# Optimization experiments

Hardware: AMD Instinct MI355X
Metric: run time of the kernel (lower is better)

## Reference

```python
import jax, jax.numpy as jnp
import numpy as np
from jax import lax

B_SZ, L, D_MODEL = 256, 4096, 4
D_STATE, D_CONV, EXPAND, OUT = 16, 4, 2, 3
D_INNER = EXPAND * D_MODEL  # 8
DT_RANK = max(1, -(-D_MODEL // 16))  # ceil(4/16) = 1


def setup_inputs() -> dict:
    key = jax.random.key(0)
    ks = jax.random.split(key, 12)
    s = 0.1
    x = jax.random.normal(ks[0], (B_SZ, L, D_MODEL), dtype=jnp.float32)
    W_in = jax.random.normal(ks[1], (2 * D_INNER, D_MODEL), jnp.float32) * s
    conv_w = jax.random.normal(ks[2], (D_INNER, 1, D_CONV), jnp.float32) * s
    conv_b = jax.random.normal(ks[3], (D_INNER,), jnp.float32) * s
    W_xproj = jax.random.normal(ks[4], (DT_RANK + 2 * D_STATE, D_INNER), jnp.float32) * s
    W_dt = jax.random.normal(ks[5], (D_INNER, DT_RANK), jnp.float32) * s
    b_dt = jax.random.normal(ks[6], (D_INNER,), jnp.float32) * s
    # standard Mamba S4D-real init: A = 1..N repeated per channel
    A_log = jnp.log(jnp.tile(jnp.arange(1, D_STATE + 1, dtype=jnp.float32)[None, :], (D_INNER, 1)))
    D = jnp.ones((D_INNER,), jnp.float32)
    W_out = jax.random.normal(ks[7], (D_MODEL, D_INNER), jnp.float32) * s
    fc_w = jax.random.normal(ks[8], (OUT, D_MODEL), jnp.float32) * s
    fc_b = jax.random.normal(ks[9], (OUT,), jnp.float32) * s
    return {"x": x, "W_in": W_in, "conv_w": conv_w, "conv_b": conv_b,
            "W_xproj": W_xproj, "W_dt": W_dt, "b_dt": b_dt, "A_log": A_log,
            "D": D, "W_out": W_out, "fc_w": fc_w, "fc_b": fc_b}


def _mamba_forward(x, W_in, conv_w, conv_b, W_xproj, W_dt, b_dt, A_log, D, W_out):
    # in_proj (no bias): (B,L,2*ed)
    xz = jnp.einsum('bld,ed->ble', x, W_in)
    xi, z = jnp.split(xz, 2, axis=-1)
    # depthwise causal conv1d over time
    xi_t = jnp.moveaxis(xi, 1, 2)  # (B, ed, L)
    xi_t = lax.conv_general_dilated(
        xi_t, conv_w, window_strides=(1,), padding=[(D_CONV - 1, 0)],
        feature_group_count=D_INNER, dimension_numbers=('NCH', 'OIH', 'NCH'))
    xi_t = xi_t + conv_b[None, :, None]
    u = jax.nn.silu(jnp.moveaxis(xi_t, 1, 2))  # (B, L, ed)
    # x_proj -> dt, B, C
    x_dbl = jnp.einsum('bld,rd->blr', u, W_xproj)
    dt_r = x_dbl[..., :DT_RANK]
    Bm = x_dbl[..., DT_RANK:DT_RANK + D_STATE]
    Cm = x_dbl[..., DT_RANK + D_STATE:]
    dt = jax.nn.softplus(jnp.einsum('blr,dr->bld', dt_r, W_dt) + b_dt)  # (B,L,ed)
    A = -jnp.exp(A_log)  # (ed, N)
    # selective scan over time
    def step(h, inp):
        dt_t, B_t, C_t, u_t = inp  # (B,ed),(B,N),(B,N),(B,ed)
        h = jnp.exp(dt_t[..., None] * A) * h + (dt_t * u_t)[..., None] * B_t[:, None, :]
        y = jnp.einsum('bdn,bn->bd', h, C_t)
        return h, y
    h0 = jnp.zeros((x.shape[0], D_INNER, D_STATE), x.dtype)
    inputs = (jnp.moveaxis(dt, 1, 0), jnp.moveaxis(Bm, 1, 0),
              jnp.moveaxis(Cm, 1, 0), jnp.moveaxis(u, 1, 0))
    _, ys = lax.scan(step, h0, inputs)  # (L,B,ed)
    y = jnp.moveaxis(ys, 0, 1) + u * D  # skip connection
    y = y * jax.nn.silu(z)
    return jnp.einsum('ble,de->bld', y, W_out)  # (B,L,d_model)


def reference(x, W_in, conv_w, conv_b, W_xproj, W_dt, b_dt, A_log, D, W_out, fc_w, fc_b):
    y = _mamba_forward(x, W_in, conv_w, conv_b, W_xproj, W_dt, b_dt, A_log, D, W_out)
    vel = jnp.einsum('bld,od->blo', y, fc_w) + fc_b  # (B,L,3)
    t = x[:, :, 0:1]
    dtm = t[:, 1:, :] - t[:, :-1, :]
    dtm = jnp.concatenate([jnp.zeros((x.shape[0], 1, 1), x.dtype), dtm], axis=1)
    return x[:, :, 1:4] + vel * dtm
```

## Files before the change

### kernel.cpp

```cpp
#include <hip/hip_runtime.h>
#include <hip/hip_fp16.h>

#define LSEQ   4096
#define SEG    1024
#define NCTOT  64
#define CLEN   64

__device__ __forceinline__ float rcpf(float v){ return __builtin_amdgcn_rcpf(v); }

template<int CTRL>
__device__ __forceinline__ float dppadd(float v){
  int r = __builtin_amdgcn_update_dpp(0, __builtin_bit_cast(int,v), CTRL, 0xF, 0xF, true);
  return v + __builtin_bit_cast(float,r);
}
__device__ __forceinline__ float quadsum(float v){
  v = dppadd<0xB1>(v);
  v = dppadd<0x4E>(v);
  return v;
}
__device__ __forceinline__ void qdt(float v, float& q, float& dt){
  float e = __expf(v);
  float qq = rcpf(1.f + e);
  q = qq;
  float d0 = -__logf(qq);
  dt = (v > 15.f) ? v : d0;
}
__device__ __forceinline__ float dot8(const float* __restrict__ w, const float* u){
  float s = 0.f;
  #pragma unroll
  for (int d=0; d<8; d++) s = fmaf(w[d], u[d], s);
  return s;
}
__device__ __forceinline__ float dot4v(const float* __restrict__ w, float4 v){
  return fmaf(w[0],v.x, fmaf(w[1],v.y, fmaf(w[2],v.z, w[3]*v.w)));
}
__device__ __forceinline__ float siluf(float v){ return v * rcpf(1.f + __expf(-v)); }

__global__ __launch_bounds__(256,4) void kA(
    const float* __restrict__ x, const float* __restrict__ W_in,
    const float* __restrict__ conv_w, const float* __restrict__ conv_b,
    const float* __restrict__ W_xproj, const float* __restrict__ W_dt,
    const float* __restrict__ b_dt,
    float* __restrict__ Ap, float* __restrict__ Hl)
{
  __shared__ float4 xs[SEG+4];
  __shared__ float2 Pl[4][16][10];
  __shared__ __half Bl[4][16][24];

  const int t = threadIdx.x;
  const int b  = blockIdx.x >> 2;
  const int qt = blockIdx.x & 3;
  const size_t base = (size_t)b*LSEQ + (size_t)qt*SEG;
  const float4* x4 = (const float4*)x;
  #pragma unroll
  for (int kk=0;kk<4;kk++) xs[3 + kk*256 + t] = x4[base + kk*256 + t];
  if (t < 3) xs[t] = (qt>0) ? x4[base - 3 + t] : make_float4(0.f,0.f,0.f,0.f);
  __syncthreads();

  const int w = t >> 6, lane = t & 63;
  const int pk = lane >> 4, pj = (lane >> 2) & 3, pp = lane & 3;
  const int sk = lane >> 4, sd = (lane >> 1) & 7, snh = lane & 1;

  float h[8]; float prun = 1.f;
  #pragma unroll
  for (int j=0;j<8;j++) h[j]=0.f;

  #pragma unroll 1
  for (int mt=0; mt<16; mt++){
    const int i0 = mt*4;
    {
      int rt = pk*4 + pj;
      int segrow = w*256 + pk*64 + i0 + pj;
      float4 v = xs[segrow + pp];
      float uu[8];
      #pragma unroll
      for (int d=0; d<8; d++){
        float xiw = dot4v(W_in + d*4, v);
        float s = quadsum(conv_w[d*4+pp] * xiw);
        uu[d] = siluf(s + conv_b[d]);
      }
      float bn[4];
      #pragma unroll
      for (int kd=0; kd<4; kd++) bn[kd] = dot8(W_xproj + (1+pp*4+kd)*8, uu);
      uint2 bw;
      ((__half2*)&bw)[0] = __floats2half2_rn(bn[0],bn[1]);
      ((__half2*)&bw)[1] = __floats2half2_rn(bn[2],bn[3]);
      *(uint2*)&Bl[w][rt][pp*4] = bw;
      float dtr = dot8(W_xproj, uu);
      int d0 = pp*2;
      float q0,dt0,q1,dt1;
      qdt(fmaf(dtr,W_dt[d0  ],b_dt[d0  ]), q0, dt0);
      qdt(fmaf(dtr,W_dt[d0+1],b_dt[d0+1]), q1, dt1);
      *(float4*)&Pl[w][rt][d0] = make_float4(q0, dt0*uu[d0], q1, dt1*uu[d0+1]);
    }
    {
      #pragma unroll
      for (int j=0;j<4;j++){
        int rt = sk*4 + j;
        float2 P = Pl[w][rt][sd];
        uint4 braw = *(uint4*)&Bl[w][rt][snh*8];
        float2 f0=__half22float2(((__half2*)&braw)[0]);
        float2 f1=__half22float2(((__half2*)&braw)[1]);
        float2 f2=__half22float2(((__half2*)&braw)[2]);
        float2 f3=__half22float2(((__half2*)&braw)[3]);
        float q=P.x, dtu=P.y;
        float q2=q*q, q4=q2*q2, q8=q4*q4;
        float p3=q2*q, p5=q4*q, p6=q4*q2, p7=p6*q;
        float m = snh ? q8 : 1.f;
        h[0]=fmaf(q *m, h[0], dtu*f0.x);
        h[1]=fmaf(q2*m, h[1], dtu*f0.y);
        h[2]=fmaf(p3*m, h[2], dtu*f1.x);
        h[3]=fmaf(q4*m, h[3], dtu*f1.y);
        h[4]=fmaf(p5*m, h[4], dtu*f2.x);
        h[5]=fmaf(p6*m, h[5], dtu*f2.y);
        h[6]=fmaf(p7*m, h[6], dtu*f3.x);
        h[7]=fmaf(q8*m, h[7], dtu*f3.y);
        prun *= q;
      }
    }
  }
  float Q=prun, Q2=Q*Q, Q4=Q2*Q2, Q8=Q4*Q4;
  float R3=Q2*Q, R5=Q4*Q, R6=Q4*Q2, R7=R6*Q;
  float M = snh ? Q8 : 1.f;
  size_t sb = ((size_t)(b*NCTOT + qt*16 + w*4 + sk))*128 + sd*16 + snh*8;
  *(float4*)&Ap[sb]   = make_float4(Q*M, Q2*M, R3*M, Q4*M);
  *(float4*)&Ap[sb+4] = make_float4(R5*M, R6*M, R7*M, Q8*M);
  *(float4*)&Hl[sb]   = make_float4(h[0],h[1],h[2],h[3]);
  *(float4*)&Hl[sb+4] = make_float4(h[4],h[5],h[6],h[7]);
}

__global__ __launch_bounds__(256) void kB(
    const float* __restrict__ Ap, const float* __restrict__ Hl,
    float* __restrict__ Hin)
{
  int g = blockIdx.x*256 + threadIdx.x;
  int b = g >> 7, e = g & 127;
  float h = 0.f;
  #pragma unroll 8
  for (int c=0; c<NCTOT; c++){
    size_t s = ((size_t)b*NCTOT + c)*128 + e;
    float a = Ap[s], hl = Hl[s];
    Hin[s] = h;
    h = fmaf(a, h, hl);
  }
}

__global__ __launch_bounds__(256,4) void kC(
    const float* __restrict__ x, const float* __restrict__ W_in,
    const float* __restrict__ conv_w, const float* __restrict__ conv_b,
    const float* __restrict__ W_xproj, const float* __restrict__ W_dt,
    const float* __restrict__ b_dt, const float* __restrict__ Dp,
    const float* __restrict__ W_out, const float* __restrict__ fc_w,
    const float* __restrict__ fc_b, const float* __restrict__ Hin,
    float* __restrict__ out)
{
  __shared__ float4  xs[SEG+4];
  __shared__ float2  Pl[4][16][10];
  __shared__ __half  BCl[4][16][40];
  __shared__ __half2 El[4][16][10];
  __shared__ float   yol[4][16][12];
  __shared__ __half  outStage[SEG*3];

  const int t = threadIdx.x;
  const int b  = blockIdx.x >> 2;
  const int qt = blockIdx.x & 3;
  const size_t base = (size_t)b*LSEQ + (size_t)qt*SEG;
  const float4* x4 = (const float4*)x;
  #pragma unroll
  for (int kk=0;kk<4;kk++) xs[3 + kk*256 + t] = x4[base + kk*256 + t];
  if (t < 3) xs[t] = (qt>0) ? x4[base - 3 + t] : make_float4(0.f,0.f,0.f,0.f);
  __syncthreads();

  const int w = t >> 6, lane = t & 63;
  const int pk = lane >> 4, pj = (lane >> 2) & 3, pp = lane & 3;
  const int sk = lane >> 4, sd = (lane >> 1) & 7, snh = lane & 1;
  const int eo = lane >> 4, err = lane & 15;

  float P2r[8]; float fb = 0.f;
  {
    int o = (eo < 3) ? eo : 0;
    #pragma unroll
    for (int d=0; d<8; d++){
      float s0 = 0.f;
      #pragma unroll
      for (int m=0;m<4;m++) s0 = fmaf(fc_w[o*4+m], W_out[m*8+d], s0);
      P2r[d] = s0;
    }
    fb = fc_b[o];
  }
  const float Dd0 = Dp[pp*2], Dd1 = Dp[pp*2+1];

  float h[8];
  {
    size_t sb = ((size_t)(b*NCTOT + qt*16 + w*4 + sk))*128 + sd*16 + snh*8;
    float4 h0 = *(const float4*)&Hin[sb];
    float4 h1 = *(const float4*)&Hin[sb+4];
    h[0]=h0.x;h[1]=h0.y;h[2]=h0.z;h[3]=h0.w;
    h[4]=h1.x;h[5]=h1.y;h[6]=h1.z;h[7]=h1.w;
  }

  #pragma unroll 1
  for (int mt=0; mt<16; mt++){
    const int i0 = mt*4;
    {
      int rt = pk*4 + pj;
      int segrow = w*256 + pk*64 + i0 + pj;
      float4 v = xs[segrow + pp];
      float uu[8];
      #pragma unroll
      for (int d=0; d<8; d++){
        float xiw = dot4v(W_in + d*4, v);
        float s = quadsum(conv_w[d*4+pp] * xiw);
        uu[d] = siluf(s + conv_b[d]);
      }
      float bn[4], cn[4];
      #pragma unroll
      for (int kd=0; kd<4; kd++){
        bn[kd] = dot8(W_xproj + ( 1+pp*4+kd)*8, uu);
        cn[kd] = dot8(W_xproj + (17+pp*4+kd)*8, uu);
      }
      uint2 bw, cw;
      ((__half2*)&bw)[0] = __floats2half2_rn(bn[0],bn[1]);
      ((__half2*)&bw)[1] = __floats2half2_rn(bn[2],bn[3]);
      ((__half2*)&cw)[0] = __floats2half2_rn(cn[0],cn[1]);
      ((__half2*)&cw)[1] = __floats2half2_rn(cn[2],cn[3]);
      *(uint2*)&BCl[w][rt][pp*4]      = bw;
      *(uint2*)&BCl[w][rt][16+pp*4]   = cw;
      float dtr = dot8(W_xproj, uu);
      float4 xc = xs[segrow + 3];
      int d0 = pp*2;
      float q0,dt0,q1,dt1;
      qdt(fmaf(dtr,W_dt[d0  ],b_dt[d0  ]), q0, dt0);
      qdt(fmaf(dtr,W_dt[d0+1],b_dt[d0+1]), q1, dt1);
      float z0 = dot4v(W_in + (8+d0  )*4, xc);
      float z1 = dot4v(W_in + (8+d0+1)*4, xc);
      float sz0 = siluf(z0), sz1 = siluf(z1);
      uint2 ew;
      ((__half2*)&ew)[0] = __floats2half2_rn(sz0, uu[d0  ]*Dd0*sz0);
      ((__half2*)&ew)[1] = __floats2half2_rn(sz1, uu[d0+1]*Dd1*sz1);
      *(uint2*)&El[w][rt][d0] = ew;
      *(float4*)&Pl[w][rt][d0] = make_float4(q0, dt0*uu[d0], q1, dt1*uu[d0+1]);
    }
    {
      #pragma unroll
      for (int j=0;j<4;j++){
        int rt = sk*4 + j;
        float2 P = Pl[w][rt][sd];
        uint4 braw = *(uint4*)&BCl[w][rt][snh*8];
        uint4 craw = *(uint4*)&BCl[w][rt][16+snh*8];
        float2 f0=__half22float2(((__half2*)&braw)[0]);
        float2 f1=__half22float2(((__half2*)&braw)[1]);
        float2 f2=__half22float2(((__half2*)&braw)[2]);
        float2 f3=__half22float2(((__half2*)&braw)[3]);
        float2 g0=__half22float2(((__half2*)&craw)[0]);
        float2 g1=__half22float2(((__half2*)&craw)[1]);
        float2 g2=__half22float2(((__half2*)&craw)[2]);
        float2 g3=__half22float2(((__half2*)&craw)[3]);
        float q=P.x, dtu=P.y;
        float q2=q*q, q4=q2*q2, q8=q4*q4;
        float p3=q2*q, p5=q4*q, p6=q4*q2, p7=p6*q;
        float m = snh ? q8 : 1.f;
        h[0]=fmaf(q *m, h[0], dtu*f0.x);
        h[1]=fmaf(q2*m, h[1], dtu*f0.y);
        h[2]=fmaf(p3*m, h[2], dtu*f1.x);
        h[3]=fmaf(q4*m, h[3], dtu*f1.y);
        h[4]=fmaf(p5*m, h[4], dtu*f2.x);
        h[5]=fmaf(p6*m, h[5], dtu*f2.y);
        h[6]=fmaf(p7*m, h[6], dtu*f3.x);
        h[7]=fmaf(q8*m, h[7], dtu*f3.y);
        float y = h[0]*g0.x;
        y = fmaf(h[1],g0.y,y); y = fmaf(h[2],g1.x,y); y = fmaf(h[3],g1.y,y);
        y = fmaf(h[4],g2.x,y); y = fmaf(h[5],g2.y,y); y = fmaf(h[6],g3.x,y);
        y = fmaf(h[7],g3.y,y);
        y = dppadd<0xB1>(y);
        if (!snh){
          float2 e = __half22float2(El[w][rt][sd]);
          yol[w][rt][sd] = fmaf(y, e.x, e.y);
        }
      }
    }
    if (lane < 48){
      int kk = err >> 2, jj = err & 3;
      float4 y0 = *(float4*)&yol[w][err][0];
      float4 y1 = *(float4*)&yol[w][err][4];
      float a = fb;
      a = fmaf(P2r[0],y0.x,a); a = fmaf(P2r[1],y0.y,a);
      a = fmaf(P2r[2],y0.z,a); a = fmaf(P2r[3],y0.w,a);
      a = fmaf(P2r[4],y1.x,a); a = fmaf(P2r[5],y1.y,a);
      a = fmaf(P2r[6],y1.z,a); a = fmaf(P2r[7],y1.w,a);
      int segrow = w*256 + kk*64 + i0 + jj;
      outStage[segrow*3 + eo] = __float2half(a);
    }
  }

  const float* xsf = (const float*)xs;
  float* outg = out + (size_t)(b*LSEQ + qt*SEG)*3;
  #pragma unroll
  for (int rep=0; rep<12; rep++){
    int gg = w*768 + rep*64 + lane;
    int row = gg/3;
    int o = gg - row*3;
    float acc = __half2float(outStage[gg]);
    float dtm = (qt==0 && row==0) ? 0.f : xsf[(3+row)*4] - xsf[(2+row)*4];
    float xc = xsf[(3+row)*4 + 1 + o];
    outg[gg] = fmaf(acc, dtm, xc);
  }
}

extern "C" void kernel_launch(void* const* d_in, const int* in_sizes, int n_in,
                              void* d_out, int out_size, void* d_ws, size_t ws_size,
                              hipStream_t stream)
{
  const float* x       = (const float*)d_in[0];
  const float* W_in    = (const float*)d_in[1];
  const float* conv_w  = (const float*)d_in[2];
  const float* conv_b  = (const float*)d_in[3];
  const float* W_xproj = (const float*)d_in[4];
  const float* W_dt    = (const float*)d_in[5];
  const float* b_dt    = (const float*)d_in[6];
  const float* Dp      = (const float*)d_in[8];
  const float* W_out   = (const float*)d_in[9];
  const float* fc_w    = (const float*)d_in[10];
  const float* fc_b    = (const float*)d_in[11];
  float* out = (float*)d_out;

  char* wsp = (char*)d_ws;
  float* Ap  = (float*)(wsp);
  float* Hl  = (float*)(wsp + (size_t)8388608);
  float* Hin = (float*)(wsp + (size_t)16777216);

  hipLaunchKernelGGL(kA, dim3(1024), dim3(256), 0, stream,
                     x, W_in, conv_w, conv_b, W_xproj, W_dt, b_dt, Ap, Hl);
  hipLaunchKernelGGL(kB, dim3(128), dim3(256), 0, stream, Ap, Hl, Hin);
  hipLaunchKernelGGL(kC, dim3(1024), dim3(256), 0, stream,
                     x, W_in, conv_w, conv_b, W_xproj, W_dt, b_dt, Dp,
                     W_out, fc_w, fc_b, Hin, out);
}
```

Before: 208.0 us.

## Halve chunk length, double grid, use packed float2 math and fp32 LDS staging

Segments shrink from 1024 to 512 timesteps and chunks from 64 to 32, so both scan kernels launch twice as many blocks and the middle chunk-carry kernel walks 128 chunks instead of 64. The per-step math is rewritten with two-wide vector types so it can map to packed FMA. The conv output is computed once per lane pair and broadcast with DPP rather than recomputed for all 8 channels per lane. B/C staging in LDS moves from half to float, and the silu(z) and D terms are stored with the dt data in one float4. The goal is more parallelism and fewer VALU instructions per step, at the cost of a longer serial carry pass, twice the workspace traffic, and more LDS per block.

```diff
diff --git a/kernel.cpp b/kernel.cpp
--- a/kernel.cpp
+++ b/kernel.cpp
@@ -2,41 +2,82 @@
 #include <hip/hip_fp16.h>
 
 #define LSEQ   4096
-#define SEG    1024
-#define NCTOT  64
-#define CLEN   64
+#define SEG    512
+#define CLEN   32
+#define NCTOT  128
+#define MTS    8
+
+typedef float v2f __attribute__((ext_vector_type(2)));
 
 __device__ __forceinline__ float rcpf(float v){ return __builtin_amdgcn_rcpf(v); }
 
 template<int CTRL>
-__device__ __forceinline__ float dppadd(float v){
-  int r = __builtin_amdgcn_update_dpp(0, __builtin_bit_cast(int,v), CTRL, 0xF, 0xF, true);
-  return v + __builtin_bit_cast(float,r);
-}
-__device__ __forceinline__ float quadsum(float v){
-  v = dppadd<0xB1>(v);
-  v = dppadd<0x4E>(v);
+__device__ __forceinline__ float dppmov(float v){
+  return __builtin_bit_cast(float, __builtin_amdgcn_update_dpp(0, __builtin_bit_cast(int,v), CTRL, 0xF, 0xF, true));
+}
+template<int CTRL>
+__device__ __forceinline__ v2f dppmov2(v2f v){
+  v2f r; r.x = dppmov<CTRL>(v.x); r.y = dppmov<CTRL>(v.y); return r;
+}
+__device__ __forceinline__ v2f fma2(v2f a, v2f b, v2f c){ return __builtin_elementwise_fma(a,b,c); }
+__device__ __forceinline__ v2f sp2(float x){ return (v2f){x,x}; }
+__device__ __forceinline__ v2f qsum2(v2f v){
+  v2f a = dppmov2<0xB1>(v); v += a;
+  v2f b2 = dppmov2<0x4E>(v); v += b2;
   return v;
 }
-__device__ __forceinline__ void qdt(float v, float& q, float& dt){
-  float e = __expf(v);
-  float qq = rcpf(1.f + e);
-  q = qq;
-  float d0 = -__logf(qq);
-  dt = (v > 15.f) ? v : d0;
-}
-__device__ __forceinline__ float dot8(const float* __restrict__ w, const float* u){
-  float s = 0.f;
-  #pragma unroll
-  for (int d=0; d<8; d++) s = fmaf(w[d], u[d], s);
-  return s;
-}
-__device__ __forceinline__ float dot4v(const float* __restrict__ w, float4 v){
-  return fmaf(w[0],v.x, fmaf(w[1],v.y, fmaf(w[2],v.z, w[3]*v.w)));
-}
-__device__ __forceinline__ float siluf(float v){ return v * rcpf(1.f + __expf(-v)); }
-
-__global__ __launch_bounds__(256,4) void kA(
+__device__ __forceinline__ v2f silu2(v2f v){
+  v2f s; s.x = rcpf(1.f+__expf(-v.x)); s.y = rcpf(1.f+__expf(-v.y));
+  return v*s;
+}
+__device__ __forceinline__ void qdt2(v2f vv, v2f& q, v2f& dt){
+  q.x = rcpf(1.f + __expf(vv.x));
+  q.y = rcpf(1.f + __expf(vv.y));
+  dt.x = (vv.x > 15.f) ? vv.x : -__logf(q.x);
+  dt.y = (vv.y > 15.f) ? vv.y : -__logf(q.y);
+}
+__device__ __forceinline__ float dot8p(const float* __restrict__ w, v2f u01, v2f u23, v2f u45, v2f u67){
+  const v2f* W = (const v2f*)w;
+  v2f a = W[0]*u01;
+  a = fma2(W[1], u23, a);
+  a = fma2(W[2], u45, a);
+  a = fma2(W[3], u67, a);
+  return a.x + a.y;
+}
+
+struct UU { v2f u01,u23,u45,u67, upair; float4 v; };
+__device__ __forceinline__ UU conv_u(const float4* __restrict__ xs, int segrow, int pp,
+    const float* __restrict__ W_in, const v2f* cwp, v2f cbp)
+{
+  float4 v = xs[segrow + pp];
+  v2f pre[4];
+  #pragma unroll
+  for (int dp=0; dp<4; dp++){
+    const float* wa = W_in + (2*dp)*4;
+    const float* wb = W_in + (2*dp+1)*4;
+    v2f a = (v2f){wa[0],wb[0]} * sp2(v.x);
+    a = fma2((v2f){wa[1],wb[1]}, sp2(v.y), a);
+    a = fma2((v2f){wa[2],wb[2]}, sp2(v.z), a);
+    a = fma2((v2f){wa[3],wb[3]}, sp2(v.w), a);
+    pre[dp] = a * cwp[dp];
+  }
+  #pragma unroll
+  for (int dp=0; dp<4; dp++) pre[dp] = qsum2(pre[dp]);
+  v2f c01 = (pp&1) ? pre[1] : pre[0];
+  v2f c23 = (pp&1) ? pre[3] : pre[2];
+  v2f own = (pp&2) ? c23 : c01;
+  own += cbp;
+  v2f up = silu2(own);
+  UU r;
+  r.u01 = dppmov2<0x00>(up);
+  r.u23 = dppmov2<0x55>(up);
+  r.u45 = dppmov2<0xAA>(up);
+  r.u67 = dppmov2<0xFF>(up);
+  r.upair = up; r.v = v;
+  return r;
+}
+
+__global__ __launch_bounds__(256,8) void kA(
     const float* __restrict__ x, const float* __restrict__ W_in,
     const float* __restrict__ conv_w, const float* __restrict__ conv_b,
     const float* __restrict__ W_xproj, const float* __restrict__ W_dt,
@@ -45,88 +86,86 @@
 {
   __shared__ float4 xs[SEG+4];
   __shared__ float2 Pl[4][16][10];
-  __shared__ __half Bl[4][16][24];
+  __shared__ float  Bs[4][16][20];
 
   const int t = threadIdx.x;
-  const int b  = blockIdx.x >> 2;
-  const int qt = blockIdx.x & 3;
+  const int b  = blockIdx.x >> 3;
+  const int qt = blockIdx.x & 7;
   const size_t base = (size_t)b*LSEQ + (size_t)qt*SEG;
   const float4* x4 = (const float4*)x;
-  #pragma unroll
-  for (int kk=0;kk<4;kk++) xs[3 + kk*256 + t] = x4[base + kk*256 + t];
+  xs[3 + t] = x4[base + t];
+  xs[3 + 256 + t] = x4[base + 256 + t];
   if (t < 3) xs[t] = (qt>0) ? x4[base - 3 + t] : make_float4(0.f,0.f,0.f,0.f);
   __syncthreads();
 
   const int w = t >> 6, lane = t & 63;
-  const int pk = lane >> 4, pj = (lane >> 2) & 3, pp = lane & 3;
-  const int sk = lane >> 4, sd = (lane >> 1) & 7, snh = lane & 1;
-
-  float h[8]; float prun = 1.f;
-  #pragma unroll
-  for (int j=0;j<8;j++) h[j]=0.f;
+  const int pk = lane>>4, pj=(lane>>2)&3, pp=lane&3;
+  const int sk = lane>>4, sd=(lane>>1)&7, snh=lane&1;
+  const int d0 = pp*2;
+
+  v2f cwp[4];
+  #pragma unroll
+  for (int dp=0;dp<4;dp++) cwp[dp] = (v2f){conv_w[(2*dp)*4+pp], conv_w[(2*dp+1)*4+pp]};
+  const v2f cbp  = (v2f){conv_b[d0], conv_b[d0+1]};
+  const v2f wdtp = (v2f){W_dt[d0], W_dt[d0+1]};
+  const v2f bdtp = (v2f){b_dt[d0], b_dt[d0+1]};
+
+  v2f h01=sp2(0.f), h23=sp2(0.f), h45=sp2(0.f), h67=sp2(0.f);
+  float prun = 1.f;
 
   #pragma unroll 1
-  for (int mt=0; mt<16; mt++){
-    const int i0 = mt*4;
+  for (int mt=0; mt<MTS; mt++){
     {
       int rt = pk*4 + pj;
-      int segrow = w*256 + pk*64 + i0 + pj;
-      float4 v = xs[segrow + pp];
-      float uu[8];
-      #pragma unroll
-      for (int d=0; d<8; d++){
-        float xiw = dot4v(W_in + d*4, v);
-        float s = quadsum(conv_w[d*4+pp] * xiw);
-        uu[d] = siluf(s + conv_b[d]);
-      }
+      int segrow = w*128 + pk*32 + mt*4 + pj;
+      UU s = conv_u(xs, segrow, pp, W_in, cwp, cbp);
       float bn[4];
       #pragma unroll
-      for (int kd=0; kd<4; kd++) bn[kd] = dot8(W_xproj + (1+pp*4+kd)*8, uu);
-      uint2 bw;
-      ((__half2*)&bw)[0] = __floats2half2_rn(bn[0],bn[1]);
-      ((__half2*)&bw)[1] = __floats2half2_rn(bn[2],bn[3]);
-      *(uint2*)&Bl[w][rt][pp*4] = bw;
-      float dtr = dot8(W_xproj, uu);
-      int d0 = pp*2;
-      float q0,dt0,q1,dt1;
-      qdt(fmaf(dtr,W_dt[d0  ],b_dt[d0  ]), q0, dt0);
-      qdt(fmaf(dtr,W_dt[d0+1],b_dt[d0+1]), q1, dt1);
-      *(float4*)&Pl[w][rt][d0] = make_float4(q0, dt0*uu[d0], q1, dt1*uu[d0+1]);
-    }
-    {
-      #pragma unroll
-      for (int j=0;j<4;j++){
-        int rt = sk*4 + j;
-        float2 P = Pl[w][rt][sd];
-        uint4 braw = *(uint4*)&Bl[w][rt][snh*8];
-        float2 f0=__half22float2(((__half2*)&braw)[0]);
-        float2 f1=__half22float2(((__half2*)&braw)[1]);
-        float2 f2=__half22float2(((__half2*)&braw)[2]);
-        float2 f3=__half22float2(((__half2*)&braw)[3]);
-        float q=P.x, dtu=P.y;
-        float q2=q*q, q4=q2*q2, q8=q4*q4;
-        float p3=q2*q, p5=q4*q, p6=q4*q2, p7=p6*q;
-        float m = snh ? q8 : 1.f;
-        h[0]=fmaf(q *m, h[0], dtu*f0.x);
-        h[1]=fmaf(q2*m, h[1], dtu*f0.y);
-        h[2]=fmaf(p3*m, h[2], dtu*f1.x);
-        h[3]=fmaf(q4*m, h[3], dtu*f1.y);
-        h[4]=fmaf(p5*m, h[4], dtu*f2.x);
-        h[5]=fmaf(p6*m, h[5], dtu*f2.y);
-        h[6]=fmaf(p7*m, h[6], dtu*f3.x);
-        h[7]=fmaf(q8*m, h[7], dtu*f3.y);
-        prun *= q;
-      }
-    }
-  }
-  float Q=prun, Q2=Q*Q, Q4=Q2*Q2, Q8=Q4*Q4;
-  float R3=Q2*Q, R5=Q4*Q, R6=Q4*Q2, R7=R6*Q;
-  float M = snh ? Q8 : 1.f;
-  size_t sb = ((size_t)(b*NCTOT + qt*16 + w*4 + sk))*128 + sd*16 + snh*8;
-  *(float4*)&Ap[sb]   = make_float4(Q*M, Q2*M, R3*M, Q4*M);
-  *(float4*)&Ap[sb+4] = make_float4(R5*M, R6*M, R7*M, Q8*M);
-  *(float4*)&Hl[sb]   = make_float4(h[0],h[1],h[2],h[3]);
-  *(float4*)&Hl[sb+4] = make_float4(h[4],h[5],h[6],h[7]);
+      for (int k2=0;k2<4;k2++)
+        bn[k2] = dot8p(W_xproj + (1+pp*4+k2)*8, s.u01,s.u23,s.u45,s.u67);
+      *(float4*)&Bs[w][rt][pp*4] = make_float4(bn[0],bn[1],bn[2],bn[3]);
+      float dtr = dot8p(W_xproj, s.u01,s.u23,s.u45,s.u67);
+      v2f q, dt;
+      qdt2(fma2(sp2(dtr), wdtp, bdtp), q, dt);
+      v2f dtu = dt * s.upair;
+      *(float4*)&Pl[w][rt][d0] = make_float4(q.x, dtu.x, q.y, dtu.y);
+    }
+    #pragma unroll
+    for (int j=0;j<4;j++){
+      int rt = sk*4 + j;
+      float2 P  = *(const float2*)&Pl[w][rt][sd];
+      float4 bA = *(const float4*)&Bs[w][rt][snh*8];
+      float4 bB = *(const float4*)&Bs[w][rt][snh*8+4];
+      float q = P.x, q2 = q*q;
+      v2f t01 = (v2f){q, q2};
+      v2f t23 = t01 * sp2(q2);
+      float q4 = t23.y;
+      v2f t45 = t01 * sp2(q4);
+      v2f t67 = t23 * sp2(q4);
+      float m = snh ? t67.y : 1.f;
+      v2f ms = sp2(m), du = sp2(P.y);
+      h01 = fma2(t01*ms, h01, du*(v2f){bA.x,bA.y});
+      h23 = fma2(t23*ms, h23, du*(v2f){bA.z,bA.w});
+      h45 = fma2(t45*ms, h45, du*(v2f){bB.x,bB.y});
+      h67 = fma2(t67*ms, h67, du*(v2f){bB.z,bB.w});
+      prun *= q;
+    }
+  }
+  float Q = prun, Q2 = Q*Q;
+  v2f s01 = (v2f){Q, Q2};
+  v2f s23 = s01 * sp2(Q2);
+  float Q4 = s23.y;
+  v2f s45 = s01 * sp2(Q4);
+  v2f s67 = s23 * sp2(Q4);
+  float M = snh ? s67.y : 1.f;
+  v2f Ms = sp2(M);
+  s01*=Ms; s23*=Ms; s45*=Ms; s67*=Ms;
+  int c = qt*16 + w*4 + sk;
+  size_t sb = ((size_t)(b*NCTOT + c))*128 + sd*16 + snh*8;
+  *(float4*)&Ap[sb]   = make_float4(s01.x,s01.y,s23.x,s23.y);
+  *(float4*)&Ap[sb+4] = make_float4(s45.x,s45.y,s67.x,s67.y);
+  *(float4*)&Hl[sb]   = make_float4(h01.x,h01.y,h23.x,h23.y);
+  *(float4*)&Hl[sb+4] = make_float4(h45.x,h45.y,h67.x,h67.y);
 }
 
 __global__ __launch_bounds__(256) void kB(
@@ -138,14 +177,14 @@
   float h = 0.f;
   #pragma unroll 8
   for (int c=0; c<NCTOT; c++){
-    size_t s = ((size_t)b*NCTOT + c)*128 + e;
+    size_t s = ((size_t)(b*NCTOT + c))*128 + e;
     float a = Ap[s], hl = Hl[s];
     Hin[s] = h;
     h = fmaf(a, h, hl);
   }
 }
 
-__global__ __launch_bounds__(256,4) void kC(
+__global__ __launch_bounds__(256,5) void kC(
     const float* __restrict__ x, const float* __restrict__ W_in,
     const float* __restrict__ conv_w, const float* __restrict__ conv_b,
     const float* __restrict__ W_xproj, const float* __restrict__ W_dt,
@@ -154,156 +193,148 @@
     const float* __restrict__ fc_b, const float* __restrict__ Hin,
     float* __restrict__ out)
 {
-  __shared__ float4  xs[SEG+4];
-  __shared__ float2  Pl[4][16][10];
-  __shared__ __half  BCl[4][16][40];
-  __shared__ __half2 El[4][16][10];
-  __shared__ float   yol[4][16][12];
-  __shared__ __half  outStage[SEG*3];
+  __shared__ float4 xs[SEG+4];
+  __shared__ float4 Pl4[4][16][9];
+  __shared__ float  BC[4][16][36];
+  __shared__ float  yol[4][16][8];
+  __shared__ __half outStage[SEG*3];
 
   const int t = threadIdx.x;
-  const int b  = blockIdx.x >> 2;
-  const int qt = blockIdx.x & 3;
+  const int b  = blockIdx.x >> 3;
+  const int qt = blockIdx.x & 7;
   const size_t base = (size_t)b*LSEQ + (size_t)qt*SEG;
   const float4* x4 = (const float4*)x;
-  #pragma unroll
-  for (int kk=0;kk<4;kk++) xs[3 + kk*256 + t] = x4[base + kk*256 + t];
+  xs[3 + t] = x4[base + t];
+  xs[3 + 256 + t] = x4[base + 256 + t];
   if (t < 3) xs[t] = (qt>0) ? x4[base - 3 + t] : make_float4(0.f,0.f,0.f,0.f);
   __syncthreads();
 
   const int w = t >> 6, lane = t & 63;
-  const int pk = lane >> 4, pj = (lane >> 2) & 3, pp = lane & 3;
-  const int sk = lane >> 4, sd = (lane >> 1) & 7, snh = lane & 1;
+  const int pk = lane>>4, pj=(lane>>2)&3, pp=lane&3;
+  const int sk = lane>>4, sd=(lane>>1)&7, snh=lane&1;
   const int eo = lane >> 4, err = lane & 15;
-
-  float P2r[8]; float fb = 0.f;
+  const int d0 = pp*2;
+
+  v2f cwp[4];
+  #pragma unroll
+  for (int dp=0;dp<4;dp++) cwp[dp] = (v2f){conv_w[(2*dp)*4+pp], conv_w[(2*dp+1)*4+pp]};
+  const v2f cbp  = (v2f){conv_b[d0], conv_b[d0+1]};
+  const v2f wdtp = (v2f){W_dt[d0], W_dt[d0+1]};
+  const v2f bdtp = (v2f){b_dt[d0], b_dt[d0+1]};
+  const v2f Dpp  = (v2f){Dp[d0], Dp[d0+1]};
+
+  v2f P2p[4]; float fb;
   {
     int o = (eo < 3) ? eo : 0;
+    float P2[8];
     #pragma unroll
     for (int d=0; d<8; d++){
       float s0 = 0.f;
       #pragma unroll
       for (int m=0;m<4;m++) s0 = fmaf(fc_w[o*4+m], W_out[m*8+d], s0);
-      P2r[d] = s0;
-    }
+      P2[d] = s0;
+    }
+    P2p[0]=(v2f){P2[0],P2[1]}; P2p[1]=(v2f){P2[2],P2[3]};
+    P2p[2]=(v2f){P2[4],P2[5]}; P2p[3]=(v2f){P2[6],P2[7]};
     fb = fc_b[o];
   }
-  const float Dd0 = Dp[pp*2], Dd1 = Dp[pp*2+1];
-
-  float h[8];
+
+  v2f h01, h23, h45, h67;
   {
-    size_t sb = ((size_t)(b*NCTOT + qt*16 + w*4 + sk))*128 + sd*16 + snh*8;
-    float4 h0 = *(const float4*)&Hin[sb];
-    float4 h1 = *(const float4*)&Hin[sb+4];
-    h[0]=h0.x;h[1]=h0.y;h[2]=h0.z;h[3]=h0.w;
-    h[4]=h1.x;h[5]=h1.y;h[6]=h1.z;h[7]=h1.w;
+    int c = qt*16 + w*4 + sk;
+    size_t sb = ((size_t)(b*NCTOT + c))*128 + sd*16 + snh*8;
+    float4 a0 = *(const float4*)&Hin[sb];
+    float4 a1 = *(const float4*)&Hin[sb+4];
+    h01=(v2f){a0.x,a0.y}; h23=(v2f){a0.z,a0.w};
+    h45=(v2f){a1.x,a1.y}; h67=(v2f){a1.z,a1.w};
   }
 
   #pragma unroll 1
-  for (int mt=0; mt<16; mt++){
-    const int i0 = mt*4;
+  for (int mt=0; mt<MTS; mt++){
     {
       int rt = pk*4 + pj;
-      int segrow = w*256 + pk*64 + i0 + pj;
-      float4 v = xs[segrow + pp];
-      float uu[8];
-      #pragma unroll
-      for (int d=0; d<8; d++){
-        float xiw = dot4v(W_in + d*4, v);
-        float s = quadsum(conv_w[d*4+pp] * xiw);
-        uu[d] = siluf(s + conv_b[d]);
-      }
+      int segrow = w*128 + pk*32 + mt*4 + pj;
+      UU s = conv_u(xs, segrow, pp, W_in, cwp, cbp);
       float bn[4], cn[4];
       #pragma unroll
-      for (int kd=0; kd<4; kd++){
-        bn[kd] = dot8(W_xproj + ( 1+pp*4+kd)*8, uu);
-        cn[kd] = dot8(W_xproj + (17+pp*4+kd)*8, uu);
+      for (int k2=0;k2<4;k2++){
+        bn[k2] = dot8p(W_xproj + ( 1+pp*4+k2)*8, s.u01,s.u23,s.u45,s.u67);
+        cn[k2] = dot8p(W_xproj + (17+pp*4+k2)*8, s.u01,s.u23,s.u45,s.u67);
       }
-      uint2 bw, cw;
-      ((__half2*)&bw)[0] = __floats2half2_rn(bn[0],bn[1]);
-      ((__half2*)&bw)[1] = __floats2half2_rn(bn[2],bn[3]);
-      ((__half2*)&cw)[0] = __floats2half2_rn(cn[0],cn[1]);
-      ((__half2*)&cw)[1] = __floats2half2_rn(cn[2],cn[3]);
-      *(uint2*)&BCl[w][rt][pp*4]      = bw;
-      *(uint2*)&BCl[w][rt][16+pp*4]   = cw;
-      float dtr = dot8(W_xproj, uu);
-      float4 xc = xs[segrow + 3];
-      int d0 = pp*2;
-      float q0,dt0,q1,dt1;
-      qdt(fmaf(dtr,W_dt[d0  ],b_dt[d0  ]), q0, dt0);
-      qdt(fmaf(dtr,W_dt[d0+1],b_dt[d0+1]), q1, dt1);
-      float z0 = dot4v(W_in + (8+d0  )*4, xc);
-      float z1 = dot4v(W_in + (8+d0+1)*4, xc);
-      float sz0 = siluf(z0), sz1 = siluf(z1);
-      uint2 ew;
-      ((__half2*)&ew)[0] = __floats2half2_rn(sz0, uu[d0  ]*Dd0*sz0);
-      ((__half2*)&ew)[1] = __floats2half2_rn(sz1, uu[d0+1]*Dd1*sz1);
-      *(uint2*)&El[w][rt][d0] = ew;
-      *(float4*)&Pl[w][rt][d0] = make_float4(q0, dt0*uu[d0], q1, dt1*uu[d0+1]);
-    }
-    {
-      #pragma unroll
-      for (int j=0;j<4;j++){
-        int rt = sk*4 + j;
-        float2 P = Pl[w][rt][sd];
-        uint4 braw = *(uint4*)&BCl[w][rt][snh*8];
-        uint4 craw = *(uint4*)&BCl[w][rt][16+snh*8];
-        float2 f0=__half22float2(((__half2*)&braw)[0]);
-        float2 f1=__half22float2(((__half2*)&braw)[1]);
-        float2 f2=__half22float2(((__half2*)&braw)[2]);
-        float2 f3=__half22float2(((__half2*)&braw)[3]);
-        float2 g0=__half22float2(((__half2*)&craw)[0]);
-        float2 g1=__half22float2(((__half2*)&craw)[1]);
-        float2 g2=__half22float2(((__half2*)&craw)[2]);
-        float2 g3=__half22float2(((__half2*)&craw)[3]);
-        float q=P.x, dtu=P.y;
-        float q2=q*q, q4=q2*q2, q8=q4*q4;
-        float p3=q2*q, p5=q4*q, p6=q4*q2, p7=p6*q;
-        float m = snh ? q8 : 1.f;
-        h[0]=fmaf(q *m, h[0], dtu*f0.x);
-        h[1]=fmaf(q2*m, h[1], dtu*f0.y);
-        h[2]=fmaf(p3*m, h[2], dtu*f1.x);
-        h[3]=fmaf(q4*m, h[3], dtu*f1.y);
-        h[4]=fmaf(p5*m, h[4], dtu*f2.x);
-        h[5]=fmaf(p6*m, h[5], dtu*f2.y);
-        h[6]=fmaf(p7*m, h[6], dtu*f3.x);
-        h[7]=fmaf(q8*m, h[7], dtu*f3.y);
-        float y = h[0]*g0.x;
-        y = fmaf(h[1],g0.y,y); y = fmaf(h[2],g1.x,y); y = fmaf(h[3],g1.y,y);
-        y = fmaf(h[4],g2.x,y); y = fmaf(h[5],g2.y,y); y = fmaf(h[6],g3.x,y);
-        y = fmaf(h[7],g3.y,y);
-        y = dppadd<0xB1>(y);
-        if (!snh){
-          float2 e = __half22float2(El[w][rt][sd]);
-          yol[w][rt][sd] = fmaf(y, e.x, e.y);
-        }
-      }
+      *(float4*)&BC[w][rt][pp*4]    = make_float4(bn[0],bn[1],bn[2],bn[3]);
+      *(float4*)&BC[w][rt][16+pp*4] = make_float4(cn[0],cn[1],cn[2],cn[3]);
+      float dtr = dot8p(W_xproj, s.u01,s.u23,s.u45,s.u67);
+      v2f q, dt;
+      qdt2(fma2(sp2(dtr), wdtp, bdtp), q, dt);
+      v2f dtu = dt * s.upair;
+      float4 xc;
+      xc.x = dppmov<0xFF>(s.v.x); xc.y = dppmov<0xFF>(s.v.y);
+      xc.z = dppmov<0xFF>(s.v.z); xc.w = dppmov<0xFF>(s.v.w);
+      const float* za = W_in + (8+d0)*4;
+      const float* zb = W_in + (9+d0)*4;
+      v2f zp = (v2f){za[0],zb[0]} * sp2(xc.x);
+      zp = fma2((v2f){za[1],zb[1]}, sp2(xc.y), zp);
+      zp = fma2((v2f){za[2],zb[2]}, sp2(xc.z), zp);
+      zp = fma2((v2f){za[3],zb[3]}, sp2(xc.w), zp);
+      v2f sz = silu2(zp);
+      v2f uD = s.upair * Dpp * sz;
+      Pl4[w][rt][d0]   = make_float4(q.x, dtu.x, sz.x, uD.x);
+      Pl4[w][rt][d0+1] = make_float4(q.y, dtu.y, sz.y, uD.y);
+    }
+    #pragma unroll
+    for (int j=0;j<4;j++){
+      int rt = sk*4 + j;
+      float4 P  = Pl4[w][rt][sd];
+      float4 bA = *(const float4*)&BC[w][rt][snh*8];
+      float4 bB = *(const float4*)&BC[w][rt][snh*8+4];
+      float4 cA = *(const float4*)&BC[w][rt][16+snh*8];
+      float4 cB = *(const float4*)&BC[w][rt][16+snh*8+4];
+      float q = P.x, q2 = q*q;
+      v2f t01 = (v2f){q, q2};
+      v2f t23 = t01 * sp2(q2);
+      float q4 = t23.y;
+      v2f t45 = t01 * sp2(q4);
+      v2f t67 = t23 * sp2(q4);
+      float m = snh ? t67.y : 1.f;
+      v2f ms = sp2(m), du = sp2(P.y);
+      h01 = fma2(t01*ms, h01, du*(v2f){bA.x,bA.y});
+      h23 = fma2(t23*ms, h23, du*(v2f){bA.z,bA.w});
+      h45 = fma2(t45*ms, h45, du*(v2f){bB.x,bB.y});
+      h67 = fma2(t67*ms, h67, du*(v2f){bB.z,bB.w});
+      v2f ya = h01*(v2f){cA.x,cA.y};
+      ya = fma2(h23, (v2f){cA.z,cA.w}, ya);
+      ya = fma2(h45, (v2f){cB.x,cB.y}, ya);
+      ya = fma2(h67, (v2f){cB.z,cB.w}, ya);
+      float y = ya.x + ya.y;
+      y += dppmov<0xB1>(y);
+      float ye = fmaf(y, P.z, P.w);
+      if (!snh) yol[w][rt][sd] = ye;
     }
     if (lane < 48){
+      float4 y0 = *(const float4*)&yol[w][err][0];
+      float4 y1 = *(const float4*)&yol[w][err][4];
+      v2f a2 = (v2f){y0.x,y0.y} * P2p[0];
+      a2 = fma2((v2f){y0.z,y0.w}, P2p[1], a2);
+      a2 = fma2((v2f){y1.x,y1.y}, P2p[2], a2);
+      a2 = fma2((v2f){y1.z,y1.w}, P2p[3], a2);
+      float a = fb + a2.x + a2.y;
       int kk = err >> 2, jj = err & 3;
-      float4 y0 = *(float4*)&yol[w][err][0];
-      float4 y1 = *(float4*)&yol[w][err][4];
-      float a = fb;
-      a = fmaf(P2r[0],y0.x,a); a = fmaf(P2r[1],y0.y,a);
-      a = fmaf(P2r[2],y0.z,a); a = fmaf(P2r[3],y0.w,a);
-      a = fmaf(P2r[4],y1.x,a); a = fmaf(P2r[5],y1.y,a);
-      a = fmaf(P2r[6],y1.z,a); a = fmaf(P2r[7],y1.w,a);
-      int segrow = w*256 + kk*64 + i0 + jj;
+      int segrow = w*128 + kk*32 + mt*4 + jj;
       outStage[segrow*3 + eo] = __float2half(a);
     }
   }
 
   const float* xsf = (const float*)xs;
-  float* outg = out + (size_t)(b*LSEQ + qt*SEG)*3;
-  #pragma unroll
-  for (int rep=0; rep<12; rep++){
-    int gg = w*768 + rep*64 + lane;
-    int row = gg/3;
-    int o = gg - row*3;
-    float acc = __half2float(outStage[gg]);
+  float* outg = out + ((size_t)(b*LSEQ + qt*SEG))*3 + w*384;
+  #pragma unroll
+  for (int rep=0; rep<6; rep++){
+    int gg = rep*64 + lane;
+    int gb = w*384 + gg;
+    int row = gb/3;
+    int o = gb - row*3;
+    float acc = __half2float(outStage[gb]);
     float dtm = (qt==0 && row==0) ? 0.f : xsf[(3+row)*4] - xsf[(2+row)*4];
-    float xc = xsf[(3+row)*4 + 1 + o];
-    outg[gg] = fmaf(acc, dtm, xc);
+    outg[gg] = fmaf(acc, dtm, xsf[(3+row)*4 + 1 + o]);
   }
 }
 
@@ -326,13 +357,13 @@
 
   char* wsp = (char*)d_ws;
   float* Ap  = (float*)(wsp);
-  float* Hl  = (float*)(wsp + (size_t)8388608);
-  float* Hin = (float*)(wsp + (size_t)16777216);
-
-  hipLaunchKernelGGL(kA, dim3(1024), dim3(256), 0, stream,
+  float* Hl  = (float*)(wsp + (size_t)16777216);
+  float* Hin = (float*)(wsp + (size_t)33554432);
+
+  hipLaunchKernelGGL(kA, dim3(2048), dim3(256), 0, stream,
                      x, W_in, conv_w, conv_b, W_xproj, W_dt, b_dt, Ap, Hl);
   hipLaunchKernelGGL(kB, dim3(128), dim3(256), 0, stream, Ap, Hl, Hin);
-  hipLaunchKernelGGL(kC, dim3(1024), dim3(256), 0, stream,
+  hipLaunchKernelGGL(kC, dim3(2048), dim3(256), 0, stream,
                      x, W_in, conv_w, conv_b, W_xproj, W_dt, b_dt, Dp,
                      W_out, fc_w, fc_b, Hin, out);
 }
```

New measurement: 315.9 us. +51.9%, slower.
